# Performance work log

Hardware: AMD Instinct MI355X
Metric: run time of the kernel (lower is better)

The kernel has to match this reference:

```python
import jax, jax.numpy as jnp
import numpy as np
import math

CH = 256
HEADS = 4
GROUPS = 8
EPS = 1e-5


def group_norm(x, gamma, beta):
    # x: [B, C, H, W], normalize over (C//G, H, W) per group
    B, C, H, W = x.shape
    xg = x.reshape(B, GROUPS, C // GROUPS, H, W)
    mean = xg.mean(axis=(2, 3, 4), keepdims=True)
    var = xg.var(axis=(2, 3, 4), keepdims=True)
    xn = ((xg - mean) * jax.lax.rsqrt(var + EPS)).reshape(B, C, H, W)
    return xn * gamma[None, :, None, None] + beta[None, :, None, None]


def setup_inputs() -> dict:
    key = jax.random.key(0)
    ks = jax.random.split(key, 7)
    B, C, H, W = 4, CH, 64, 64
    x = jax.random.normal(ks[0], (B, C, H, W), dtype=jnp.float32)
    norm_w = jnp.ones((C,), dtype=jnp.float32)
    norm_b = jnp.zeros((C,), dtype=jnp.float32)
    s = 1.0 / math.sqrt(C)
    qkv_w = jax.random.normal(ks[1], (3 * C, C), dtype=jnp.float32) * s  # 1x1 conv kernel
    qkv_b = jnp.zeros((3 * C,), dtype=jnp.float32)
    proj_w = jax.random.normal(ks[2], (C, C), dtype=jnp.float32) * s
    proj_b = jnp.zeros((C,), dtype=jnp.float32)
    return {"x": x, "norm_w": norm_w, "norm_b": norm_b,
            "qkv_w": qkv_w, "qkv_b": qkv_b,
            "proj_w": proj_w, "proj_b": proj_b}


def reference(x, norm_w, norm_b, qkv_w, qkv_b, proj_w, proj_b):
    B, C, H, W = x.shape
    d = C // HEADS
    h = group_norm(x, norm_w, norm_b)
    # 1x1 conv == channel matmul
    qkv = jnp.einsum('oc,bchw->bohw', qkv_w, h) + qkv_b[None, :, None, None]
    qkv = qkv.reshape(B, 3, HEADS, d, H * W)
    q, k, v = qkv[:, 0], qkv[:, 1], qkv[:, 2]  # [B, heads, d, HW]
    attn = jnp.einsum('bhdi,bhdj->bhij', q, k) / jnp.sqrt(jnp.float32(d))
    attn = jax.nn.softmax(attn, axis=-1)
    out = jnp.einsum('bhij,bhdj->bhdi', attn, v).reshape(B, C, H, W)
    out = jnp.einsum('oc,bchw->bohw', proj_w, out) + proj_b[None, :, None, None]
    return x + out
```

## Files before the change

kernel.cpp:

```cpp
#include <hip/hip_runtime.h>
#include <stdint.h>

#define NB    4
#define CC    256
#define NN    4096
#define NHEAD 4
#define DH    64
#define NGRP  8
#define GSIZE 131072

typedef unsigned short u16;
typedef __attribute__((ext_vector_type(8))) short s16x8;
typedef __attribute__((ext_vector_type(4))) float f32x4;

__device__ __forceinline__ u16 f2b(float f) {
  uint32_t x = __float_as_uint(f);
  x += 0x7fffu + ((x >> 16) & 1u);
  return (u16)(x >> 16);
}

__device__ __forceinline__ uint32_t pk2(float a, float b) {
  uint32_t r;
  asm("v_cvt_pk_bf16_f32 %0, %1, %2" : "=v"(r) : "v"(a), "v"(b));
  return r;
}

__global__ __launch_bounds__(256) void k_prep(const float* __restrict__ qw,
                                              const float* __restrict__ pw,
                                              u16* __restrict__ qwb,
                                              u16* __restrict__ pwb,
                                              float* __restrict__ stats) {
  int i = blockIdx.x * 256 + threadIdx.x;
  if (i < 64) stats[i] = 0.f;
  for (int idx = i; idx < 3 * CC * CC; idx += 65536) qwb[idx] = f2b(qw[idx]);
  if (i < CC * CC) pwb[i] = f2b(pw[i]);
}

__global__ __launch_bounds__(256) void k_gn_stats(const float* __restrict__ x,
                                                  float* __restrict__ stats) {
  int grp = blockIdx.x >> 4, sub = blockIdx.x & 15;
  const float4* p4 = (const float4*)(x + (size_t)grp * GSIZE + (size_t)sub * 8192);
  float s = 0.f, s2 = 0.f;
#pragma unroll
  for (int i = 0; i < 8; ++i) {
    float4 v = p4[threadIdx.x + 256 * i];
    s  += v.x + v.y + v.z + v.w;
    s2 += v.x * v.x + v.y * v.y + v.z * v.z + v.w * v.w;
  }
#pragma unroll
  for (int off = 1; off < 64; off <<= 1) { s += __shfl_xor(s, off); s2 += __shfl_xor(s2, off); }
  __shared__ float red[8];
  int w = threadIdx.x >> 6;
  if ((threadIdx.x & 63) == 0) { red[w] = s; red[4 + w] = s2; }
  __syncthreads();
  if (threadIdx.x == 0) {
    s  = red[0] + red[1] + red[2] + red[3];
    s2 = red[4] + red[5] + red[6] + red[7];
    atomicAdd(&stats[grp], s);
    atomicAdd(&stats[32 + grp], s2);
  }
}

__global__ __launch_bounds__(256) void k_gn_norm(const float* __restrict__ x,
                                                 const float* __restrict__ stats,
                                                 const float* __restrict__ gw,
                                                 const float* __restrict__ gb,
                                                 u16* __restrict__ ht) {
  __shared__ u16 T[64 * 72];
  int b = blockIdx.z, cb = blockIdx.y, nb = blockIdx.x;
  int t = threadIdx.x;
  int c = t >> 2, nch = (t & 3) * 16;
  int cg = cb * 64 + c;
  int grp = b * NGRP + (cg >> 5);
  float mean = stats[grp] * (1.f / (float)GSIZE);
  float var  = stats[32 + grp] * (1.f / (float)GSIZE) - mean * mean;
  float rstd = rsqrtf(var + 1e-5f);
  float ga = gw[cg] * rstd;
  float be = gb[cg] - mean * ga;
  const float* px = x + ((size_t)b * CC + cg) * NN + nb * 64 + nch;
#pragma unroll
  for (int k = 0; k < 4; ++k) {
    float4 v = *(const float4*)(px + 4 * k);
    int nl = nch + 4 * k;
    T[(nl + 0) * 72 + c] = f2b(v.x * ga + be);
    T[(nl + 1) * 72 + c] = f2b(v.y * ga + be);
    T[(nl + 2) * 72 + c] = f2b(v.z * ga + be);
    T[(nl + 3) * 72 + c] = f2b(v.w * ga + be);
  }
  __syncthreads();
  int n = t >> 2, cch = (t & 3) * 16;
  u16* dst = ht + ((size_t)b * NN + nb * 64 + n) * CC + cb * 64 + cch;
  *(uint4*)(dst)     = *(const uint4*)&T[n * 72 + cch];
  *(uint4*)(dst + 8) = *(const uint4*)&T[n * 72 + cch + 8];
}

__global__ __launch_bounds__(256) void k_qkv(const u16* __restrict__ Aw,
                                             const float* __restrict__ bias,
                                             const u16* __restrict__ ht,
                                             u16* __restrict__ Qt,
                                             u16* __restrict__ Kt,
                                             u16* __restrict__ Vv) {
  __shared__ u16 sm[5120];
  u16* As = sm;
  u16* Bs = sm + 2560;
  int b = blockIdx.z, bm = blockIdx.y, bn = blockIdx.x;
  int t = threadIdx.x, w = t >> 6, lane = t & 63, lr = lane & 15, lg = lane >> 4;
  int wm = w >> 1, wn = w & 1;
  int srow = t >> 2, sch = (t & 3) * 8;
  const u16* Ap = Aw + (size_t)(bm * 64 + srow) * CC + sch;
  const u16* Bp = ht + ((size_t)b * NN + bn * 64 + srow) * CC + sch;
  f32x4 acc[2][2] = {};
  for (int kt = 0; kt < CC / 32; ++kt) {
    *(uint4*)&As[srow * 40 + sch] = *(const uint4*)(Ap + kt * 32);
    *(uint4*)&Bs[srow * 40 + sch] = *(const uint4*)(Bp + kt * 32);
    __syncthreads();
    s16x8 af[2], bf[2];
#pragma unroll
    for (int fm = 0; fm < 2; ++fm) af[fm] = *(const s16x8*)&As[(wm * 32 + fm * 16 + lr) * 40 + lg * 8];
#pragma unroll
    for (int fn = 0; fn < 2; ++fn) bf[fn] = *(const s16x8*)&Bs[(wn * 32 + fn * 16 + lr) * 40 + lg * 8];
#pragma unroll
    for (int fm = 0; fm < 2; ++fm)
#pragma unroll
      for (int fn = 0; fn < 2; ++fn)
        acc[fm][fn] = __builtin_amdgcn_mfma_f32_16x16x32_bf16(af[fm], bf[fn], acc[fm][fn], 0, 0, 0);
    __syncthreads();
  }
  int which = bm >> 2, head = bm & 3;
  if (which == 2) {
#pragma unroll
    for (int fm = 0; fm < 2; ++fm)
#pragma unroll
      for (int fn = 0; fn < 2; ++fn)
#pragma unroll
        for (int r = 0; r < 4; ++r) {
          int m = wm * 32 + fm * 16 + lg * 4 + r;
          int n = wn * 32 + fn * 16 + lr;
          float v = acc[fm][fn][r] + bias[bm * 64 + m];
          Vv[((size_t)(b * NHEAD + head) * DH + m) * NN + bn * 64 + n] = f2b(v);
        }
  } else {
    u16* Ts = sm;
    float scale = (which == 0) ? 0.125f * 1.44269504f : 1.0f;
#pragma unroll
    for (int fm = 0; fm < 2; ++fm)
#pragma unroll
      for (int fn = 0; fn < 2; ++fn)
#pragma unroll
        for (int r = 0; r < 4; ++r) {
          int m = wm * 32 + fm * 16 + lg * 4 + r;
          int n = wn * 32 + fn * 16 + lr;
          float v = (acc[fm][fn][r] + bias[bm * 64 + m]) * scale;
          Ts[n * 72 + m] = f2b(v);
        }
    __syncthreads();
    u16* dst = (which == 0 ? Qt : Kt);
    int n = t >> 2, cch = (t & 3) * 16;
    u16* o = dst + ((size_t)(b * NHEAD + head) * NN + bn * 64 + n) * DH + cch;
    *(uint4*)(o)     = *(const uint4*)&Ts[n * 72 + cch];
    *(uint4*)(o + 8) = *(const uint4*)&Ts[n * 72 + cch + 8];
  }
}

__global__ __launch_bounds__(256, 4) void k_attn(const u16* __restrict__ Qt,
                                                 const u16* __restrict__ Kt,
                                                 const u16* __restrict__ Vv,
                                                 u16* __restrict__ att) {
  __shared__ __align__(16) u16 Ks[64 * 72];
  __shared__ __align__(16) u16 Vs[64 * 72];
  int bh = blockIdx.y, qt = blockIdx.x;
  int t = threadIdx.x, w = t >> 6, lane = t & 63, lr = lane & 15, lg = lane >> 4;
  const u16* Qb = Qt + ((size_t)bh * NN + qt * 64 + w * 16) * DH;
  const u16* Kb = Kt + (size_t)bh * NN * DH;
  const u16* Vb = Vv + (size_t)bh * DH * NN;
  s16x8 bq[2];
#pragma unroll
  for (int kk = 0; kk < 2; ++kk) bq[kk] = *(const s16x8*)(Qb + lr * DH + kk * 32 + lg * 8);
  float m = -1e30f, l = 0.f;
  f32x4 oacc[4] = {};
  int srow = t >> 2, sch = (t & 3) * 16;
  int prow = (srow & 32) | (((srow >> 2) & 3) << 3) | (((srow >> 4) & 1) << 2) | (srow & 3);
  const u16* kp0 = Kb + (size_t)prow * DH + sch;
  const u16* vp0 = Vb + (size_t)srow * NN + sch;
  uint4 rk0 = *(const uint4*)(kp0), rk1 = *(const uint4*)(kp0 + 8);
  uint4 rv0 = *(const uint4*)(vp0), rv1 = *(const uint4*)(vp0 + 8);
  *(uint4*)&Ks[srow * 72 + sch]     = rk0;
  *(uint4*)&Ks[srow * 72 + sch + 8] = rk1;
  *(uint4*)&Vs[srow * 72 + sch]     = rv0;
  *(uint4*)&Vs[srow * 72 + sch + 8] = rv1;
  __syncthreads();
  for (int j0 = 0; j0 < NN; j0 += 64) {
    int jn = (j0 + 64 < NN) ? j0 + 64 : 0;
    const u16* kp = kp0 + (size_t)jn * DH;
    const u16* vp = vp0 + jn;
    rk0 = *(const uint4*)(kp);  rk1 = *(const uint4*)(kp + 8);
    rv0 = *(const uint4*)(vp);  rv1 = *(const uint4*)(vp + 8);
    f32x4 s[4];
#pragma unroll
    for (int jt = 0; jt < 4; ++jt) {
      f32x4 z = {};
      s16x8 a0 = *(const s16x8*)&Ks[(jt * 16 + lr) * 72 + lg * 8];
      s16x8 a1 = *(const s16x8*)&Ks[(jt * 16 + lr) * 72 + 32 + lg * 8];
      z = __builtin_amdgcn_mfma_f32_16x16x32_bf16(a0, bq[0], z, 0, 0, 0);
      z = __builtin_amdgcn_mfma_f32_16x16x32_bf16(a1, bq[1], z, 0, 0, 0);
      s[jt] = z;
    }
    float mx = s[0][0];
#pragma unroll
    for (int jt = 0; jt < 4; ++jt)
#pragma unroll
      for (int r = 0; r < 4; ++r) mx = fmaxf(mx, s[jt][r]);
    mx = fmaxf(mx, __shfl_xor(mx, 16));
    mx = fmaxf(mx, __shfl_xor(mx, 32));
    if (__any(mx > m + 8.f)) {
      float mnew  = fmaxf(m, mx);
      float alpha = exp2f(m - mnew);
      l *= alpha;
#pragma unroll
      for (int dt = 0; dt < 4; ++dt)
#pragma unroll
        for (int r = 0; r < 4; ++r) oacc[dt][r] *= alpha;
      m = mnew;
    }
    float p[4][4];
    float rs = 0.f;
#pragma unroll
    for (int jt = 0; jt < 4; ++jt)
#pragma unroll
      for (int r = 0; r < 4; ++r) {
        float pv = exp2f(s[jt][r] - m);
        p[jt][r] = pv;
        rs += pv;
      }
    rs += __shfl_xor(rs, 16);
    rs += __shfl_xor(rs, 32);
    l += rs;
    union { s16x8 v; uint32_t u[4]; } pb0, pb1;
    pb0.u[0] = pk2(p[0][0], p[0][1]); pb0.u[1] = pk2(p[0][2], p[0][3]);
    pb0.u[2] = pk2(p[1][0], p[1][1]); pb0.u[3] = pk2(p[1][2], p[1][3]);
    pb1.u[0] = pk2(p[2][0], p[2][1]); pb1.u[1] = pk2(p[2][2], p[2][3]);
    pb1.u[2] = pk2(p[3][0], p[3][1]); pb1.u[3] = pk2(p[3][2], p[3][3]);
#pragma unroll
    for (int dt = 0; dt < 4; ++dt) {
      s16x8 av0 = *(const s16x8*)&Vs[(dt * 16 + lr) * 72 + lg * 8];
      s16x8 av1 = *(const s16x8*)&Vs[(dt * 16 + lr) * 72 + 32 + lg * 8];
      oacc[dt] = __builtin_amdgcn_mfma_f32_16x16x32_bf16(av0, pb0.v, oacc[dt], 0, 0, 0);
      oacc[dt] = __builtin_amdgcn_mfma_f32_16x16x32_bf16(av1, pb1.v, oacc[dt], 0, 0, 0);
    }
    __syncthreads();
    *(uint4*)&Ks[srow * 72 + sch]     = rk0;
    *(uint4*)&Ks[srow * 72 + sch + 8] = rk1;
    *(uint4*)&Vs[srow * 72 + sch]     = rv0;
    *(uint4*)&Vs[srow * 72 + sch + 8] = rv1;
    __syncthreads();
  }
  float linv = 1.f / l;
  int b = bh >> 2, h = bh & 3;
  u16* ob = att + ((size_t)b * NN + qt * 64 + w * 16 + lr) * CC + h * 64 + lg * 4;
#pragma unroll
  for (int dt = 0; dt < 4; ++dt) {
    uint2 pkd;
    pkd.x = pk2(oacc[dt][0] * linv, oacc[dt][1] * linv);
    pkd.y = pk2(oacc[dt][2] * linv, oacc[dt][3] * linv);
    *(uint2*)(ob + dt * 16) = pkd;
  }
}

__global__ __launch_bounds__(256) void k_proj(const u16* __restrict__ Aw,
                                              const float* __restrict__ bias,
                                              const u16* __restrict__ att,
                                              const float* __restrict__ x,
                                              float* __restrict__ out) {
  __shared__ u16 sm[5120];
  u16* As = sm;
  u16* Bs = sm + 2560;
  int b = blockIdx.z, bm = blockIdx.y, bn = blockIdx.x;
  int t = threadIdx.x, w = t >> 6, lane = t & 63, lr = lane & 15, lg = lane >> 4;
  int wm = w >> 1, wn = w & 1;
  int srow = t >> 2, sch = (t & 3) * 8;
  const u16* Ap = Aw + (size_t)(bm * 64 + srow) * CC + sch;
  const u16* Bp = att + ((size_t)b * NN + bn * 64 + srow) * CC + sch;
  f32x4 acc[2][2] = {};
  for (int kt = 0; kt < CC / 32; ++kt) {
    *(uint4*)&As[srow * 40 + sch] = *(const uint4*)(Ap + kt * 32);
    *(uint4*)&Bs[srow * 40 + sch] = *(const uint4*)(Bp + kt * 32);
    __syncthreads();
    s16x8 af[2], bf[2];
#pragma unroll
    for (int fm = 0; fm < 2; ++fm) af[fm] = *(const s16x8*)&As[(wm * 32 + fm * 16 + lr) * 40 + lg * 8];
#pragma unroll
    for (int fn = 0; fn < 2; ++fn) bf[fn] = *(const s16x8*)&Bs[(wn * 32 + fn * 16 + lr) * 40 + lg * 8];
#pragma unroll
    for (int fm = 0; fm < 2; ++fm)
#pragma unroll
      for (int fn = 0; fn < 2; ++fn)
        acc[fm][fn] = __builtin_amdgcn_mfma_f32_16x16x32_bf16(af[fm], bf[fn], acc[fm][fn], 0, 0, 0);
    __syncthreads();
  }
#pragma unroll
  for (int fm = 0; fm < 2; ++fm)
#pragma unroll
    for (int fn = 0; fn < 2; ++fn)
#pragma unroll
      for (int r = 0; r < 4; ++r) {
        int o = bm * 64 + wm * 32 + fm * 16 + lg * 4 + r;
        int n = bn * 64 + wn * 32 + fn * 16 + lr;
        size_t idx = ((size_t)b * CC + o) * NN + n;
        out[idx] = x[idx] + bias[o] + acc[fm][fn][r];
      }
}

extern "C" void kernel_launch(void* const* d_in, const int* in_sizes, int n_in,
                              void* d_out, int out_size, void* d_ws, size_t ws_size,
                              hipStream_t stream) {
  const float* x  = (const float*)d_in[0];
  const float* nw = (const float*)d_in[1];
  const float* nb = (const float*)d_in[2];
  const float* qw = (const float*)d_in[3];
  const float* qb = (const float*)d_in[4];
  const float* pw = (const float*)d_in[5];
  const float* pb = (const float*)d_in[6];
  float* out = (float*)d_out;
  char* ws = (char*)d_ws;
  float* stats = (float*)(ws + 0);
  u16* qwb = (u16*)(ws + 4096);
  u16* pwb = (u16*)(ws + 397312);
  u16* ht  = (u16*)(ws + 528384);
  u16* Qt  = (u16*)(ws + 8916992);
  u16* Kt  = (u16*)(ws + 17305600);
  u16* Vv  = (u16*)(ws + 25694208);
  u16* att = (u16*)(ws + 34082816);

  k_prep<<<dim3(256), dim3(256), 0, stream>>>(qw, pw, qwb, pwb, stats);
  k_gn_stats<<<dim3(512), dim3(256), 0, stream>>>(x, stats);
  k_gn_norm<<<dim3(64, 4, NB), dim3(256), 0, stream>>>(x, stats, nw, nb, ht);
  k_qkv<<<dim3(64, 12, NB), dim3(256), 0, stream>>>(qwb, qb, ht, Qt, Kt, Vv);
  k_attn<<<dim3(64, NB * NHEAD), dim3(256), 0, stream>>>(Qt, Kt, Vv, att);
  k_proj<<<dim3(64, 4, NB), dim3(256), 0, stream>>>(pwb, pb, att, x, out);
}
```

Baseline: 177.8 us.

## Widen attention KV tile to 128 and compute row sums via MFMA

Doubles the key/value tile processed per loop iteration in the flash-attention kernel, halving the number of barriers and softmax max/rescale checks per query block. Replaces the shuffle-based row-sum of probabilities with an MFMA against a ones vector, so the normalizer is accumulated on the matrix unit using the same bf16-rounded probabilities. Adds s_setprio hints around MFMA sections. It increases LDS use and register pressure (8 score fragments, 8 prefetch registers), which may reduce occupancy under the launch bound of 4.

```diff
diff --git a/kernel.cpp b/kernel.cpp
--- a/kernel.cpp
+++ b/kernel.cpp
@@ -166,8 +166,8 @@
                                                  const u16* __restrict__ Kt,
                                                  const u16* __restrict__ Vv,
                                                  u16* __restrict__ att) {
-  __shared__ __align__(16) u16 Ks[64 * 72];
-  __shared__ __align__(16) u16 Vs[64 * 72];
+  __shared__ __align__(16) u16 Ks[128 * 72];
+  __shared__ __align__(16) u16 Vs[64 * 136];
   int bh = blockIdx.y, qt = blockIdx.x;
   int t = threadIdx.x, w = t >> 6, lane = t & 63, lr = lane & 15, lg = lane >> 4;
   const u16* Qb = Qt + ((size_t)bh * NN + qt * 64 + w * 16) * DH;
@@ -176,85 +176,99 @@
   s16x8 bq[2];
 #pragma unroll
   for (int kk = 0; kk < 2; ++kk) bq[kk] = *(const s16x8*)(Qb + lr * DH + kk * 32 + lg * 8);
-  float m = -1e30f, l = 0.f;
+  const s16x8 ones = (s16x8)(short)0x3F80;
+  float m = -1e30f;
   f32x4 oacc[4] = {};
-  int srow = t >> 2, sch = (t & 3) * 16;
-  int prow = (srow & 32) | (((srow >> 2) & 3) << 3) | (((srow >> 4) & 1) << 2) | (srow & 3);
-  const u16* kp0 = Kb + (size_t)prow * DH + sch;
-  const u16* vp0 = Vb + (size_t)srow * NN + sch;
-  uint4 rk0 = *(const uint4*)(kp0), rk1 = *(const uint4*)(kp0 + 8);
-  uint4 rv0 = *(const uint4*)(vp0), rv1 = *(const uint4*)(vp0 + 8);
-  *(uint4*)&Ks[srow * 72 + sch]     = rk0;
-  *(uint4*)&Ks[srow * 72 + sch + 8] = rk1;
-  *(uint4*)&Vs[srow * 72 + sch]     = rv0;
-  *(uint4*)&Vs[srow * 72 + sch + 8] = rv1;
+  f32x4 lacc = {};
+  int srK = t >> 1, scK = (t & 1) * 32;
+  int wK = srK & 63;
+  int prK = (srK & 64) | (wK & 32) | (((wK >> 2) & 3) << 3) | (((wK >> 4) & 1) << 2) | (wK & 3);
+  const u16* kp0 = Kb + (size_t)prK * DH + scK;
+  u16* ksw = &Ks[srK * 72 + scK];
+  int srV = t >> 2, scV = (t & 3) * 32;
+  const u16* vp0 = Vb + (size_t)srV * NN + scV;
+  u16* vsw = &Vs[srV * 136 + scV];
+  {
+    uint4 a0 = *(const uint4*)(kp0),      a1 = *(const uint4*)(kp0 + 8);
+    uint4 a2 = *(const uint4*)(kp0 + 16), a3 = *(const uint4*)(kp0 + 24);
+    uint4 b0 = *(const uint4*)(vp0),      b1 = *(const uint4*)(vp0 + 8);
+    uint4 b2 = *(const uint4*)(vp0 + 16), b3 = *(const uint4*)(vp0 + 24);
+    *(uint4*)(ksw) = a0; *(uint4*)(ksw + 8) = a1; *(uint4*)(ksw + 16) = a2; *(uint4*)(ksw + 24) = a3;
+    *(uint4*)(vsw) = b0; *(uint4*)(vsw + 8) = b1; *(uint4*)(vsw + 16) = b2; *(uint4*)(vsw + 24) = b3;
+  }
   __syncthreads();
-  for (int j0 = 0; j0 < NN; j0 += 64) {
-    int jn = (j0 + 64 < NN) ? j0 + 64 : 0;
+  for (int j0 = 0; j0 < NN; j0 += 128) {
+    int jn = (j0 + 128 < NN) ? j0 + 128 : 0;
     const u16* kp = kp0 + (size_t)jn * DH;
     const u16* vp = vp0 + jn;
-    rk0 = *(const uint4*)(kp);  rk1 = *(const uint4*)(kp + 8);
-    rv0 = *(const uint4*)(vp);  rv1 = *(const uint4*)(vp + 8);
-    f32x4 s[4];
-#pragma unroll
-    for (int jt = 0; jt < 4; ++jt) {
+    uint4 rka = *(const uint4*)(kp),      rkb = *(const uint4*)(kp + 8);
+    uint4 rkc = *(const uint4*)(kp + 16), rkd = *(const uint4*)(kp + 24);
+    uint4 rva = *(const uint4*)(vp),      rvb = *(const uint4*)(vp + 8);
+    uint4 rvc = *(const uint4*)(vp + 16), rvd = *(const uint4*)(vp + 24);
+    f32x4 s[8];
+    __builtin_amdgcn_s_setprio(1);
+#pragma unroll
+    for (int q = 0; q < 8; ++q) {
+      const u16* base = &Ks[(q * 16 + lr) * 72 + lg * 8];
+      s16x8 a0 = *(const s16x8*)(base);
+      s16x8 a1 = *(const s16x8*)(base + 32);
       f32x4 z = {};
-      s16x8 a0 = *(const s16x8*)&Ks[(jt * 16 + lr) * 72 + lg * 8];
-      s16x8 a1 = *(const s16x8*)&Ks[(jt * 16 + lr) * 72 + 32 + lg * 8];
       z = __builtin_amdgcn_mfma_f32_16x16x32_bf16(a0, bq[0], z, 0, 0, 0);
       z = __builtin_amdgcn_mfma_f32_16x16x32_bf16(a1, bq[1], z, 0, 0, 0);
-      s[jt] = z;
-    }
-    float mx = s[0][0];
-#pragma unroll
-    for (int jt = 0; jt < 4; ++jt)
-#pragma unroll
-      for (int r = 0; r < 4; ++r) mx = fmaxf(mx, s[jt][r]);
+      s[q] = z;
+    }
+    __builtin_amdgcn_s_setprio(0);
+    float mx = fmaxf(s[0][0], s[0][1]);
+    mx = fmaxf(mx, fmaxf(s[0][2], s[0][3]));
+#pragma unroll
+    for (int q = 1; q < 8; ++q) {
+      mx = fmaxf(mx, fmaxf(s[q][0], s[q][1]));
+      mx = fmaxf(mx, fmaxf(s[q][2], s[q][3]));
+    }
     mx = fmaxf(mx, __shfl_xor(mx, 16));
     mx = fmaxf(mx, __shfl_xor(mx, 32));
     if (__any(mx > m + 8.f)) {
       float mnew  = fmaxf(m, mx);
       float alpha = exp2f(m - mnew);
-      l *= alpha;
 #pragma unroll
       for (int dt = 0; dt < 4; ++dt)
 #pragma unroll
         for (int r = 0; r < 4; ++r) oacc[dt][r] *= alpha;
+#pragma unroll
+      for (int r = 0; r < 4; ++r) lacc[r] *= alpha;
       m = mnew;
     }
-    float p[4][4];
-    float rs = 0.f;
-#pragma unroll
-    for (int jt = 0; jt < 4; ++jt)
-#pragma unroll
-      for (int r = 0; r < 4; ++r) {
-        float pv = exp2f(s[jt][r] - m);
-        p[jt][r] = pv;
-        rs += pv;
+    union { s16x8 v; uint32_t u[4]; } pb[4];
+#pragma unroll
+    for (int q = 0; q < 8; ++q) {
+      float p0 = exp2f(s[q][0] - m);
+      float p1 = exp2f(s[q][1] - m);
+      float p2 = exp2f(s[q][2] - m);
+      float p3 = exp2f(s[q][3] - m);
+      int c = (q >> 2) * 2 + ((q >> 1) & 1);
+      pb[c].u[(q & 1) * 2]     = pk2(p0, p1);
+      pb[c].u[(q & 1) * 2 + 1] = pk2(p2, p3);
+    }
+    __builtin_amdgcn_s_setprio(1);
+#pragma unroll
+    for (int dt = 0; dt < 4; ++dt) {
+      const u16* vb2 = &Vs[(dt * 16 + lr) * 136 + lg * 8];
+#pragma unroll
+      for (int c = 0; c < 4; ++c) {
+        s16x8 av = *(const s16x8*)(vb2 + c * 32);
+        oacc[dt] = __builtin_amdgcn_mfma_f32_16x16x32_bf16(av, pb[c].v, oacc[dt], 0, 0, 0);
       }
-    rs += __shfl_xor(rs, 16);
-    rs += __shfl_xor(rs, 32);
-    l += rs;
-    union { s16x8 v; uint32_t u[4]; } pb0, pb1;
-    pb0.u[0] = pk2(p[0][0], p[0][1]); pb0.u[1] = pk2(p[0][2], p[0][3]);
-    pb0.u[2] = pk2(p[1][0], p[1][1]); pb0.u[3] = pk2(p[1][2], p[1][3]);
-    pb1.u[0] = pk2(p[2][0], p[2][1]); pb1.u[1] = pk2(p[2][2], p[2][3]);
-    pb1.u[2] = pk2(p[3][0], p[3][1]); pb1.u[3] = pk2(p[3][2], p[3][3]);
-#pragma unroll
-    for (int dt = 0; dt < 4; ++dt) {
-      s16x8 av0 = *(const s16x8*)&Vs[(dt * 16 + lr) * 72 + lg * 8];
-      s16x8 av1 = *(const s16x8*)&Vs[(dt * 16 + lr) * 72 + 32 + lg * 8];
-      oacc[dt] = __builtin_amdgcn_mfma_f32_16x16x32_bf16(av0, pb0.v, oacc[dt], 0, 0, 0);
-      oacc[dt] = __builtin_amdgcn_mfma_f32_16x16x32_bf16(av1, pb1.v, oacc[dt], 0, 0, 0);
-    }
-    __syncthreads();
-    *(uint4*)&Ks[srow * 72 + sch]     = rk0;
-    *(uint4*)&Ks[srow * 72 + sch + 8] = rk1;
-    *(uint4*)&Vs[srow * 72 + sch]     = rv0;
-    *(uint4*)&Vs[srow * 72 + sch + 8] = rv1;
-    __syncthreads();
-  }
-  float linv = 1.f / l;
+    }
+#pragma unroll
+    for (int c = 0; c < 4; ++c)
+      lacc = __builtin_amdgcn_mfma_f32_16x16x32_bf16(ones, pb[c].v, lacc, 0, 0, 0);
+    __builtin_amdgcn_s_setprio(0);
+    __syncthreads();
+    *(uint4*)(ksw) = rka; *(uint4*)(ksw + 8) = rkb; *(uint4*)(ksw + 16) = rkc; *(uint4*)(ksw + 24) = rkd;
+    *(uint4*)(vsw) = rva; *(uint4*)(vsw + 8) = rvb; *(uint4*)(vsw + 16) = rvc; *(uint4*)(vsw + 24) = rvd;
+    __syncthreads();
+  }
+  float linv = 1.f / lacc[0];
   int b = bh >> 2, h = bh & 3;
   u16* ob = att + ((size_t)b * NN + qt * 64 + w * 16 + lr) * CC + h * 64 + lg * 4;
 #pragma unroll
```

Result: no change. 175.8 us (-1.1%).
